# Performance work log

Hardware: AMD Instinct MI355X
Metric: run time of the kernel (lower is better)

## Reference

```python
import jax, jax.numpy as jnp
import numpy as np

B, T = 4096, 16384
KLEN = 50          # min(50, n_steps) with dt=1
REFRACTORY = 3.0   # self.refractory / self.dt


def setup_inputs() -> dict:
    key = jax.random.key(0)
    k1, = jax.random.split(key, 1)
    # scale so that v_reset + I_filtered/100 can cross v_th (=-55 vs reset -70)
    I_input = jax.random.normal(k1, (B, T), dtype=jnp.float32) * 2000.0
    return {
        "I_input": I_input,
        "tau_m": jnp.float32(10.0),
        "tau_s": jnp.float32(5.0),
        "v_th": jnp.float32(-55.0),
        "v_reset": jnp.float32(-70.0),
        "eta": jnp.float32(-5.0),
    }


def _srm_spikes(I_input, tau_m, tau_s, v_th, v_reset, eta):
    # synaptic kernel: (exp(-t/tau_m) - exp(-t/tau_s)) / sum
    t = jnp.arange(KLEN, dtype=jnp.float32)
    kernel = jnp.exp(-t / tau_m) - jnp.exp(-t / tau_s)
    kernel = kernel / (jnp.sum(kernel) + 1e-10)
    # 'same' convolution per trace (np.convolve semantics: kernel flipped)
    I_filt = jax.vmap(lambda x: jnp.convolve(x, kernel, mode="same"))(I_input)

    def step(ref, I_t):
        # ref: [B] refractory countdown; I_t: [B] filtered current at time t
        in_ref = ref > 0
        v_free = v_reset + I_t / 100.0
        spike = jnp.where(jnp.logical_and(~in_ref, v_free >= v_th), 1.0, 0.0)
        new_ref = jnp.where(in_ref, ref - 1.0,
                            jnp.where(spike > 0, REFRACTORY, 0.0))
        return new_ref, spike

    ref0 = jnp.zeros((I_input.shape[0],), dtype=jnp.float32)
    # original loop runs t = 1 .. n_steps-1; spikes[0] stays 0
    _, spikes_t = jax.lax.scan(step, ref0, jnp.swapaxes(I_filt[:, 1:], 0, 1))
    spikes = jnp.concatenate(
        [jnp.zeros((I_input.shape[0], 1), dtype=jnp.float32),
         jnp.swapaxes(spikes_t, 0, 1)], axis=1)
    return spikes


def reference(I_input, tau_m, tau_s, v_th, v_reset, eta):
    return _srm_spikes(I_input, tau_m, tau_s, v_th, v_reset, eta)
```

## Files before the change

kernel.cpp:

```cpp
#include <hip/hip_runtime.h>


#define TLEN  16384
#define NROWS 4096
#define GRP   256
#define NGRP  64
#define KLEN  50
#define WPB   4
#define TILEW 336

typedef float f4 __attribute__((ext_vector_type(4)));

__device__ __forceinline__ float uniformf(float x) {
    return __int_as_float(__builtin_amdgcn_readfirstlane(__float_as_int(x)));
}

__device__ __forceinline__ int map_compose(int first, int then) {
    int r = 0;
#pragma unroll
    for (int s = 0; s < 4; ++s) {
        int a = (first >> (2 * s)) & 3;
        int b = (then >> (2 * a)) & 3;
        r |= b << (2 * s);
    }
    return r;
}

__device__ float solve_thresh(float v_reset, float v_th) {
    auto tokey = [](float f) {
        unsigned u = __float_as_uint(f);
        return (u & 0x80000000u) ? ~u : (u | 0x80000000u);
    };
    auto fromkey = [](unsigned k) {
        unsigned u = (k & 0x80000000u) ? (k & 0x7FFFFFFFu) : ~k;
        return __uint_as_float(u);
    };
    const float maxf = 3.402823466e38f;
    unsigned lo = tokey(-maxf), hi = tokey(maxf);
    if (!((v_reset + maxf / 100.0f) >= v_th))
        return __uint_as_float(0x7F800000u);
    while (lo < hi) {
        unsigned mid = lo + ((hi - lo) >> 1);
        float a = fromkey(mid);
        if ((v_reset + a / 100.0f) >= v_th) hi = mid;
        else lo = mid + 1;
    }
    return fromkey(lo);
}

__global__ __launch_bounds__(256)
void srm_kernel(const float* __restrict__ I,
                const float* __restrict__ p_tau_m,
                const float* __restrict__ p_tau_s,
                const float* __restrict__ p_v_th,
                const float* __restrict__ p_v_reset,
                float* __restrict__ out)
{
    __shared__ __align__(16) float tile[WPB][2][TILEW];

    const int lane = threadIdx.x & 63;
    const int wid  = threadIdx.x >> 6;
    const int row  = blockIdx.x * WPB + wid;

    const float tau_m   = p_tau_m[0];
    const float tau_s   = p_tau_s[0];
    const float v_th    = p_v_th[0];
    const float v_reset = p_v_reset[0];

    float ku[KLEN];
    float ksum = 0.0f;
#pragma unroll
    for (int t = 0; t < KLEN; ++t) {
        float ft = (float)t;
        float v = expf(-ft / tau_m) - expf(-ft / tau_s);
        ksum += v;
        ku[t] = uniformf(v);
    }
    const float kden = uniformf(ksum + 1e-10f);
    float kt[KLEN];
#pragma unroll
    for (int t = 0; t < KLEN; ++t) kt[t] = uniformf(ku[t] / kden);

    const float athr = uniformf(solve_thresh(v_reset, v_th));

    const float* Irow = I + (size_t)row * TLEN;
    float* Orow = out + (size_t)row * TLEN;

    float Cv[4], Nv[4], Lv[4];
    {
        f4 a = *(const f4*)(Irow + 0 * GRP + 4 * lane);
        Cv[0] = a.x; Cv[1] = a.y; Cv[2] = a.z; Cv[3] = a.w;
        f4 c = *(const f4*)(Irow + 1 * GRP + 4 * lane);
        Nv[0] = c.x; Nv[1] = c.y; Nv[2] = c.z; Nv[3] = c.w;
    }

    if (lane < 8) {
        f4 z = (f4){0.0f, 0.0f, 0.0f, 0.0f};
        *(f4*)&tile[wid][0][4 * lane] = z;
    }
    {
        f4 c; c.x = Cv[0]; c.y = Cv[1]; c.z = Cv[2]; c.w = Cv[3];
        *(f4*)&tile[wid][0][32 + 4 * lane] = c;
    }

    int r0 = 0;

    for (int g = 0; g < NGRP; ++g) {
        const int cur = g & 1;
        const int nxt = cur ^ 1;

        if (g + 2 < NGRP) {
            f4 a = __builtin_nontemporal_load(
                (const f4*)(Irow + (size_t)(g + 2) * GRP + 4 * lane));
            Lv[0] = a.x; Lv[1] = a.y; Lv[2] = a.z; Lv[3] = a.w;
        } else {
            Lv[0] = Lv[1] = Lv[2] = Lv[3] = 0.0f;
        }

        f4 nv; nv.x = Nv[0]; nv.y = Nv[1]; nv.z = Nv[2]; nv.w = Nv[3];
        if (lane < 8)
            *(f4*)&tile[wid][cur][288 + 4 * lane] = nv;
        *(f4*)&tile[wid][nxt][32 + 4 * lane] = nv;
        if (lane >= 56) {
            f4 cv; cv.x = Cv[0]; cv.y = Cv[1]; cv.z = Cv[2]; cv.w = Cv[3];
            *(f4*)&tile[wid][nxt][4 * (lane - 56)] = cv;
        }

        f4 wv[15];
#pragma unroll
        for (int i = 0; i < 15; ++i)
            wv[i] = *(const f4*)&tile[wid][cur][4 * lane + 4 + 4 * i];
#define WIN(m) (wv[(m) >> 2][(m) & 3])

        float acc[4];
        acc[0] = acc[1] = acc[2] = acc[3] = 0.0f;
#pragma unroll
        for (int o = -25; o <= 27; ++o) {
            const float w = WIN(o + 28);
#pragma unroll
            for (int k = 0; k < 4; ++k) {
                const int jj = k + 24 - o;
                if (jj >= 0 && jj < KLEN)
                    acc[k] = fmaf(kt[jj], w, acc[k]);
            }
        }
#undef WIN

        const int tb = g * GRP + 4 * lane;
        int cand[4];
#pragma unroll
        for (int k = 0; k < 4; ++k)
            cand[k] = (acc[k] >= athr) ? 1 : 0;
        cand[0] &= (tb != 0);

        const int cm = cand[0] | cand[1] | cand[2] | cand[3];
        const unsigned long long anyc = __ballot(cm != 0);

        f4 o0;
        if (anyc == 0ULL) {
            o0 = (f4){0.0f, 0.0f, 0.0f, 0.0f};
            r0 = 0;
        } else {
            int s0 = 0, s1 = 1, s2 = 2, s3 = 3;
#pragma unroll
            for (int k = 0; k < 4; ++k) {
                const int c3 = cand[k] ? 3 : 0;
                s0 = (s0 > 0) ? (s0 - 1) : c3;
                s1 = (s1 > 0) ? (s1 - 1) : c3;
                s2 = (s2 > 0) ? (s2 - 1) : c3;
                s3 = (s3 > 0) ? (s3 - 1) : c3;
            }
            int P = s0 | (s1 << 2) | (s2 << 4) | (s3 << 6);

#pragma unroll
            for (int d = 1; d < 64; d <<= 1) {
                const int prev = __shfl_up(P, d, 64);
                const int comp = map_compose(prev, P);
                P = (lane >= d) ? comp : P;
            }
            const int Pprev = __shfl_up(P, 1, 64);
            const int sin0  = (lane == 0) ? r0 : ((Pprev >> (2 * r0)) & 3);
            const int Pfull = __shfl(P, 63, 64);
            r0 = (Pfull >> (2 * r0)) & 3;

            int s = sin0;
            float sp[4];
#pragma unroll
            for (int k = 0; k < 4; ++k) {
                const int spike = (s == 0) & cand[k];
                sp[k] = spike ? 1.0f : 0.0f;
                s = (s > 0) ? (s - 1) : (cand[k] ? 3 : 0);
            }
            o0.x = sp[0]; o0.y = sp[1]; o0.z = sp[2]; o0.w = sp[3];
        }

        __builtin_nontemporal_store(o0, (f4*)(Orow + tb));

#pragma unroll
        for (int j = 0; j < 4; ++j) { Cv[j] = Nv[j]; Nv[j] = Lv[j]; }
    }
}

extern "C" void kernel_launch(void* const* d_in, const int* in_sizes, int n_in,
                              void* d_out, int out_size, void* d_ws, size_t ws_size,
                              hipStream_t stream) {
    const float* I       = (const float*)d_in[0];
    const float* tau_m   = (const float*)d_in[1];
    const float* tau_s   = (const float*)d_in[2];
    const float* v_th    = (const float*)d_in[3];
    const float* v_reset = (const float*)d_in[4];
    float* out = (float*)d_out;

    srm_kernel<<<dim3(NROWS / WPB), dim3(256), 0, stream>>>(
        I, tau_m, tau_s, v_th, v_reset, out);
}
```

Measured before the change: 158.2 us.

## Split convolution into per-row chunks and defer refractory scan to fixup kernel

The fused per-row kernel is split into two kernels. The first computes the convolution over two independent half-row chunks per row, doubling the number of waves, and writes raw threshold candidates plus a per-chunk flag to workspace. A second kernel re-reads the output only for rows that have any candidate and applies the sequential refractory scan. This gains parallelism and latency hiding for the convolution. The cost is a second launch and an extra read and write of the output for flagged rows, which with this input scale is likely most rows. The old single kernel is kept as a fallback when the workspace is too small.

Result: slower. 211.8 us (+33.9%).

```diff
diff --git a/kernel.cpp b/kernel.cpp
--- a/kernel.cpp
+++ b/kernel.cpp
@@ -8,6 +8,10 @@
 #define KLEN  50
 #define WPB   4
 #define TILEW 336
+#define CHK   2
+#define GPC   (NGRP / CHK)
+
+#define WS_NEED ((size_t)NROWS * CHK * sizeof(int))
 
 typedef float f4 __attribute__((ext_vector_type(4)));
 
@@ -49,6 +53,195 @@
 }
 
 __global__ __launch_bounds__(256)
+void conv_kernel(const float* __restrict__ I,
+                 const float* __restrict__ p_tau_m,
+                 const float* __restrict__ p_tau_s,
+                 const float* __restrict__ p_v_th,
+                 const float* __restrict__ p_v_reset,
+                 float* __restrict__ out,
+                 int* __restrict__ flags)
+{
+    __shared__ __align__(16) float tile[WPB][2][TILEW];
+
+    const int lane  = threadIdx.x & 63;
+    const int wid   = threadIdx.x >> 6;
+    const int w     = blockIdx.x * WPB + wid;
+    const int row   = w >> 1;
+    const int chunk = w & 1;
+    const int gi0   = chunk * GPC;
+
+    const float tau_m   = p_tau_m[0];
+    const float tau_s   = p_tau_s[0];
+    const float v_th    = p_v_th[0];
+    const float v_reset = p_v_reset[0];
+
+    float ku[KLEN];
+    float ksum = 0.0f;
+#pragma unroll
+    for (int t = 0; t < KLEN; ++t) {
+        float ft = (float)t;
+        float v = expf(-ft / tau_m) - expf(-ft / tau_s);
+        ksum += v;
+        ku[t] = uniformf(v);
+    }
+    const float kden = uniformf(ksum + 1e-10f);
+    float kt[KLEN];
+#pragma unroll
+    for (int t = 0; t < KLEN; ++t) kt[t] = uniformf(ku[t] / kden);
+
+    const float athr = uniformf(solve_thresh(v_reset, v_th));
+
+    const float* Irow = I + (size_t)row * TLEN;
+    float* Orow = out + (size_t)row * TLEN;
+
+    float Cv[4], Nv[4], Lv[4];
+    {
+        f4 a = *(const f4*)(Irow + (size_t)gi0 * GRP + 4 * lane);
+        Cv[0] = a.x; Cv[1] = a.y; Cv[2] = a.z; Cv[3] = a.w;
+        f4 c = *(const f4*)(Irow + (size_t)(gi0 + 1) * GRP + 4 * lane);
+        Nv[0] = c.x; Nv[1] = c.y; Nv[2] = c.z; Nv[3] = c.w;
+    }
+
+    if (lane < 8) {
+        f4 h;
+        if (chunk == 0) h = (f4){0.0f, 0.0f, 0.0f, 0.0f};
+        else            h = *(const f4*)(Irow + (size_t)gi0 * GRP - 32 + 4 * lane);
+        *(f4*)&tile[wid][0][4 * lane] = h;
+    }
+    {
+        f4 c; c.x = Cv[0]; c.y = Cv[1]; c.z = Cv[2]; c.w = Cv[3];
+        *(f4*)&tile[wid][0][32 + 4 * lane] = c;
+    }
+
+    int rowflag = 0;
+
+    for (int g = 0; g < GPC; ++g) {
+        const int cur = g & 1;
+        const int nxt = cur ^ 1;
+        const int gi  = gi0 + g;
+
+        if (gi + 2 < NGRP) {
+            f4 a = __builtin_nontemporal_load(
+                (const f4*)(Irow + (size_t)(gi + 2) * GRP + 4 * lane));
+            Lv[0] = a.x; Lv[1] = a.y; Lv[2] = a.z; Lv[3] = a.w;
+        } else {
+            Lv[0] = Lv[1] = Lv[2] = Lv[3] = 0.0f;
+        }
+
+        f4 nv; nv.x = Nv[0]; nv.y = Nv[1]; nv.z = Nv[2]; nv.w = Nv[3];
+        if (lane < 8)
+            *(f4*)&tile[wid][cur][288 + 4 * lane] = nv;
+        *(f4*)&tile[wid][nxt][32 + 4 * lane] = nv;
+        if (lane >= 56) {
+            f4 cv; cv.x = Cv[0]; cv.y = Cv[1]; cv.z = Cv[2]; cv.w = Cv[3];
+            *(f4*)&tile[wid][nxt][4 * (lane - 56)] = cv;
+        }
+
+        f4 wv[15];
+#pragma unroll
+        for (int i = 0; i < 15; ++i)
+            wv[i] = *(const f4*)&tile[wid][cur][4 * lane + 4 + 4 * i];
+#define WIN(m) (wv[(m) >> 2][(m) & 3])
+
+        float acc[4];
+        acc[0] = acc[1] = acc[2] = acc[3] = 0.0f;
+#pragma unroll
+        for (int o = -25; o <= 27; ++o) {
+            const float w2 = WIN(o + 28);
+#pragma unroll
+            for (int k = 0; k < 4; ++k) {
+                const int jj = k + 24 - o;
+                if (jj >= 0 && jj < KLEN)
+                    acc[k] = fmaf(kt[jj], w2, acc[k]);
+            }
+        }
+#undef WIN
+
+        const int tb = gi * GRP + 4 * lane;
+        int cand[4];
+#pragma unroll
+        for (int k = 0; k < 4; ++k)
+            cand[k] = (acc[k] >= athr) ? 1 : 0;
+        cand[0] &= (tb != 0);
+
+        rowflag |= cand[0] | cand[1] | cand[2] | cand[3];
+
+        f4 o0;
+        o0.x = cand[0] ? 1.0f : 0.0f;
+        o0.y = cand[1] ? 1.0f : 0.0f;
+        o0.z = cand[2] ? 1.0f : 0.0f;
+        o0.w = cand[3] ? 1.0f : 0.0f;
+        __builtin_nontemporal_store(o0, (f4*)(Orow + tb));
+
+#pragma unroll
+        for (int j = 0; j < 4; ++j) { Cv[j] = Nv[j]; Nv[j] = Lv[j]; }
+    }
+
+    const unsigned long long anyb = __ballot(rowflag != 0);
+    if (lane == 0) flags[w] = (anyb != 0ULL) ? 1 : 0;
+}
+
+__global__ __launch_bounds__(256)
+void fixup_kernel(const int* __restrict__ flags,
+                  float* __restrict__ out)
+{
+    const int lane = threadIdx.x & 63;
+    const int wid  = threadIdx.x >> 6;
+    const int row  = blockIdx.x * WPB + wid;
+
+    if ((flags[2 * row] | flags[2 * row + 1]) == 0) return;
+
+    float* Orow = out + (size_t)row * TLEN;
+    int r0 = 0;
+
+    for (int g = 0; g < NGRP; ++g) {
+        f4 o = *(const f4*)(Orow + g * GRP + 4 * lane);
+        int cand[4];
+        cand[0] = (o.x != 0.0f);
+        cand[1] = (o.y != 0.0f);
+        cand[2] = (o.z != 0.0f);
+        cand[3] = (o.w != 0.0f);
+
+        const int cm = cand[0] | cand[1] | cand[2] | cand[3];
+        const unsigned long long anyc = __ballot(cm != 0);
+        if (anyc == 0ULL) { r0 = 0; continue; }
+
+        int s0 = 0, s1 = 1, s2 = 2, s3 = 3;
+#pragma unroll
+        for (int k = 0; k < 4; ++k) {
+            const int c3 = cand[k] ? 3 : 0;
+            s0 = (s0 > 0) ? (s0 - 1) : c3;
+            s1 = (s1 > 0) ? (s1 - 1) : c3;
+            s2 = (s2 > 0) ? (s2 - 1) : c3;
+            s3 = (s3 > 0) ? (s3 - 1) : c3;
+        }
+        int P = s0 | (s1 << 2) | (s2 << 4) | (s3 << 6);
+
+#pragma unroll
+        for (int d = 1; d < 64; d <<= 1) {
+            const int prev = __shfl_up(P, d, 64);
+            const int comp = map_compose(prev, P);
+            P = (lane >= d) ? comp : P;
+        }
+        const int Pprev = __shfl_up(P, 1, 64);
+        const int sin0  = (lane == 0) ? r0 : ((Pprev >> (2 * r0)) & 3);
+        const int Pfull = __shfl(P, 63, 64);
+        r0 = (Pfull >> (2 * r0)) & 3;
+
+        int s = sin0;
+        float sp[4];
+#pragma unroll
+        for (int k = 0; k < 4; ++k) {
+            const int spike = (s == 0) & cand[k];
+            sp[k] = spike ? 1.0f : 0.0f;
+            s = (s > 0) ? (s - 1) : (cand[k] ? 3 : 0);
+        }
+        f4 o0; o0.x = sp[0]; o0.y = sp[1]; o0.z = sp[2]; o0.w = sp[3];
+        *(f4*)(Orow + g * GRP + 4 * lane) = o0;
+    }
+}
+
+__global__ __launch_bounds__(256)
 void srm_kernel(const float* __restrict__ I,
                 const float* __restrict__ p_tau_m,
                 const float* __restrict__ p_tau_s,
@@ -171,7 +364,6 @@
                 s3 = (s3 > 0) ? (s3 - 1) : c3;
             }
             int P = s0 | (s1 << 2) | (s2 << 4) | (s3 << 6);
-
 #pragma unroll
             for (int d = 1; d < 64; d <<= 1) {
                 const int prev = __shfl_up(P, d, 64);
@@ -211,6 +403,13 @@
     const float* v_reset = (const float*)d_in[4];
     float* out = (float*)d_out;
 
-    srm_kernel<<<dim3(NROWS / WPB), dim3(256), 0, stream>>>(
-        I, tau_m, tau_s, v_th, v_reset, out);
-}
+    if (ws_size >= WS_NEED) {
+        int* flags = (int*)d_ws;
+        conv_kernel<<<dim3(NROWS * CHK / WPB), dim3(256), 0, stream>>>(
+            I, tau_m, tau_s, v_th, v_reset, out, flags);
+        fixup_kernel<<<dim3(NROWS / WPB), dim3(256), 0, stream>>>(flags, out);
+    } else {
+        srm_kernel<<<dim3(NROWS / WPB), dim3(256), 0, stream>>>(
+            I, tau_m, tau_s, v_th, v_reset, out);
+    }
+}
```
